# Performance work log

Measured on AMD Instinct MI355X. Metric: run time of the kernel, lower is better.

## Reference

```python
import jax, jax.numpy as jnp
import numpy as np

N = 50000      # nodes
E = 800000     # edges (avg degree 16)
IN = 512       # input features
OUT = 32       # per-head hidden features
H = 8          # heads (layer 1)
C = 16         # classes (layer 2, 1 head)
NEG_SLOPE = 0.2


def setup_inputs() -> dict:
    key = jax.random.key(0)
    ks = jax.random.split(key, 8)
    x = jax.random.normal(ks[0], (N, IN), jnp.float32)
    edge_index = jax.random.randint(ks[1], (2, E), 0, N, jnp.int32)
    # layer 1 params: W1 [IN, H*OUT], attention vectors a1_src/a1_dst [H, OUT]
    W1 = jax.random.normal(ks[2], (IN, H * OUT), jnp.float32) * (1.0 / np.sqrt(IN))
    a1_src = jax.random.normal(ks[3], (H, OUT), jnp.float32) * (1.0 / np.sqrt(OUT))
    a1_dst = jax.random.normal(ks[4], (H, OUT), jnp.float32) * (1.0 / np.sqrt(OUT))
    # layer 2 params: single head, W2 [H*OUT, C], a2_src/a2_dst [1, C]
    W2 = jax.random.normal(ks[5], (H * OUT, C), jnp.float32) * (1.0 / np.sqrt(H * OUT))
    a2_src = jax.random.normal(ks[6], (1, C), jnp.float32) * (1.0 / np.sqrt(C))
    a2_dst = jax.random.normal(ks[7], (1, C), jnp.float32) * (1.0 / np.sqrt(C))
    return {"x": x, "W1": W1, "a1_src": a1_src, "a1_dst": a1_dst,
            "W2": W2, "a2_src": a2_src, "a2_dst": a2_dst,
            "edge_index": edge_index}


def gat_layer(x, edge_index, W, a_src, a_dst, concat):
    """Standard GAT layer: e_ij = LeakyReLU(a_src.Wh_i + a_dst.Wh_j),
    softmax over incoming edges of each target node, scatter-aggregate."""
    n = x.shape[0]
    h_heads, f = a_src.shape
    h = (x @ W).reshape(n, h_heads, f)                      # [N, H, F]
    src, dst = edge_index[0], edge_index[1]
    es = jnp.einsum('nhf,hf->nh', h, a_src)                 # [N, H] per-node src scores
    ed = jnp.einsum('nhf,hf->nh', h, a_dst)                 # [N, H]
    e = jax.nn.leaky_relu(es[src] + ed[dst], NEG_SLOPE)     # [E, H] per-edge logits
    # segment softmax over edges grouped by dst node
    m = jax.ops.segment_max(e, dst, num_segments=n)         # [N, H]
    m = jnp.where(jnp.isfinite(m), m, 0.0)                  # empty segments -> -inf
    p = jnp.exp(e - m[dst])                                 # [E, H]
    s = jax.ops.segment_sum(p, dst, num_segments=n)         # [N, H]
    denom = s[dst]
    alpha = p / jnp.where(denom > 0, denom, 1.0)            # [E, H]
    msg = h[src] * alpha[:, :, None]                        # [E, H, F]
    out = jax.ops.segment_sum(msg, dst, num_segments=n)     # [N, H, F]
    if concat:
        return out.reshape(n, h_heads * f)
    return out.mean(axis=1)


def reference(x, W1, a1_src, a1_dst, W2, a2_src, a2_dst, edge_index):
    # dropout is identity in eval mode
    h = gat_layer(x, edge_index, W1, a1_src, a1_dst, concat=True)   # [N, H*OUT]
    h = jax.nn.elu(h)
    h = gat_layer(h, edge_index, W2, a2_src, a2_dst, concat=False)  # [N, C]
    return jax.nn.log_softmax(h, axis=1)
```

## Files before the change

kernel.cpp:

```cpp
#include <hip/hip_runtime.h>

#define NN 50000
#define EE 800000
#define KIN 512
#define HF 256
#define NH 8
#define FOUT 32
#define NC 16
#define NEG 0.2f
#define NB_SCAN 196

typedef unsigned short u16;
typedef __attribute__((ext_vector_type(8))) short shortx8;
typedef __attribute__((ext_vector_type(4))) float floatx4;
typedef __attribute__((ext_vector_type(8))) unsigned short ushortx8;
typedef __attribute__((ext_vector_type(4))) unsigned uintx4;

__device__ __forceinline__ float lrelu(float x) { return x > 0.f ? x : NEG * x; }

__device__ __forceinline__ u16 f2bf(float f) {
    unsigned u = __float_as_uint(f);
    return (u16)((u + 0x7FFFu + ((u >> 16) & 1u)) >> 16);
}
__device__ __forceinline__ float bf2f(u16 v) {
    return __uint_as_float((unsigned)v << 16);
}
__device__ __forceinline__ unsigned pk2bf(float a, float b) {
    unsigned ua = __float_as_uint(a), ub = __float_as_uint(b);
    return ((ua + 0x8000u) >> 16) | ((ub + 0x8000u) & 0xffff0000u);
}

__device__ __forceinline__ void gll16(const void* g, void* l) {
    __builtin_amdgcn_global_load_lds((const __attribute__((address_space(1))) void*)g,
                                     (__attribute__((address_space(3))) void*)l, 16, 0, 0);
}

__global__ void count_deg_convw(const int* __restrict__ dst, int* __restrict__ deg,
                                const float* __restrict__ W1, const float* __restrict__ W2,
                                u16* __restrict__ w1t, u16* __restrict__ w2t) {
    int e = blockIdx.x * 256 + threadIdx.x;
    if (e < EE) atomicAdd(&deg[dst[e]], 1);
    if (e < KIN * HF) {
        int k = e >> 8, n = e & 255;
        w1t[n * KIN + k] = f2bf(W1[e]);
    } else if (e < KIN * HF + HF * NC) {
        int e2 = e - KIN * HF;
        int k = e2 >> 4, c = e2 & 15;
        w2t[c * HF + k] = f2bf(W2[e2]);
    }
}

__global__ __launch_bounds__(256) void scan_a(const int* __restrict__ deg, int* __restrict__ bsum) {
    __shared__ int sm[256];
    int t = threadIdx.x;
    int i = blockIdx.x * 256 + t;
    sm[t] = (i < NN) ? deg[i] : 0;
    __syncthreads();
    for (int o = 128; o; o >>= 1) { if (t < o) sm[t] += sm[t + o]; __syncthreads(); }
    if (t == 0) bsum[blockIdx.x] = sm[0];
}

__global__ __launch_bounds__(256) void scan_c(const int* __restrict__ deg, const int* __restrict__ bsum,
                                              int* __restrict__ off) {
    __shared__ int sm[256];
    __shared__ int pre[256];
    int t = threadIdx.x;
    pre[t] = (t < blockIdx.x && t < NB_SCAN) ? bsum[t] : 0;
    __syncthreads();
    for (int o = 128; o; o >>= 1) { if (t < o) pre[t] += pre[t + o]; __syncthreads(); }
    int bofs = pre[0];
    __syncthreads();
    int i = blockIdx.x * 256 + t;
    int d = (i < NN) ? deg[i] : 0;
    sm[t] = d;
    __syncthreads();
    for (int dd = 1; dd < 256; dd <<= 1) {
        int v = (t >= dd) ? sm[t - dd] : 0;
        __syncthreads();
        sm[t] += v;
        __syncthreads();
    }
    if (i < NN) off[i] = bofs + sm[t] - d;
    if (i == 0) off[NN] = EE;
}

__global__ void fill_csr(const int* __restrict__ src, const int* __restrict__ dst,
                         const int* __restrict__ off, int* __restrict__ cursor,
                         int* __restrict__ csr_src) {
    int e = blockIdx.x * 256 + threadIdx.x;
    if (e < EE) {
        int d = dst[e];
        int pos = atomicAdd(&cursor[d], 1);
        csr_src[off[d] + pos] = src[e];
    }
}

__global__ __launch_bounds__(256, 3) void gemm1_mfma(const float* __restrict__ x,
                                                     const u16* __restrict__ w1t,
                                                     u16* __restrict__ h1b,
                                                     const float* __restrict__ a1s,
                                                     const float* __restrict__ a1d,
                                                     float* __restrict__ es1,
                                                     float* __restrict__ ed1) {
    __shared__ __align__(16) float As0[8 * 64 * 4];
    __shared__ __align__(16) float As1[8 * 64 * 4];
    __shared__ __align__(16) u16 Bs0[4 * 256 * 8];
    __shared__ __align__(16) u16 Bs1[4 * 256 * 8];
    int t = threadIdx.x;
    int lane = t & 63, wave = t >> 6;
    int wm = wave >> 1, wn = wave & 1;
    int lm = lane & 15, quad = lane >> 4;
    int bm = blockIdx.x * 64;

    floatx4 acc[2][8];
#pragma unroll
    for (int i = 0; i < 2; i++)
#pragma unroll
        for (int j = 0; j < 8; j++) acc[i][j] = (floatx4){0.f, 0.f, 0.f, 0.f};

    int arow = bm + lane;
    if (arow > NN - 1) arow = NN - 1;
    const float* axp = x + (size_t)arow * KIN;
    const u16* bxp[4];
#pragma unroll
    for (int b = 0; b < 4; b++) bxp[b] = w1t + (size_t)(b * 64 + lane) * KIN + wave * 8;

#define G1_STAGE(AB, BB, KK)                                             \
    {                                                                    \
        _Pragma("unroll") for (int a = 0; a < 2; a++) {                  \
            int g = wave * 2 + a;                                        \
            gll16(axp + (KK) + g * 4, &AB[g * 64 * 4]);                  \
        }                                                                \
        _Pragma("unroll") for (int b = 0; b < 4; b++)                    \
            gll16(bxp[b] + (KK), &BB[(wave * 256 + b * 64) * 8]);        \
    }

#define G1_WAITV(n) do { asm volatile("s_waitcnt vmcnt(" #n ")" ::: "memory"); \
                         __builtin_amdgcn_sched_barrier(0); } while (0)
#define G1_BAR() do { __builtin_amdgcn_sched_barrier(0);                 \
                      __builtin_amdgcn_s_barrier();                      \
                      __builtin_amdgcn_sched_barrier(0); } while (0)

#define G1_COMPUTE(AB, BB)                                               \
    {                                                                    \
        shortx8 af[2], bfv[8];                                           \
        _Pragma("unroll") for (int i = 0; i < 2; i++) {                  \
            int row = wm * 32 + i * 16 + lm;                             \
            int g0 = quad * 2;                                           \
            float4 lo = *(const float4*)&AB[(g0 * 64 + row) * 4];        \
            float4 hi = *(const float4*)&AB[((g0 + 1) * 64 + row) * 4];  \
            union { uintx4 u; shortx8 s; } cv;                           \
            cv.u[0] = pk2bf(lo.x, lo.y);                                 \
            cv.u[1] = pk2bf(lo.z, lo.w);                                 \
            cv.u[2] = pk2bf(hi.x, hi.y);                                 \
            cv.u[3] = pk2bf(hi.z, hi.w);                                 \
            af[i] = cv.s;                                                \
        }                                                                \
        _Pragma("unroll") for (int j = 0; j < 8; j++) {                  \
            int col = wn * 128 + j * 16 + lm;                            \
            bfv[j] = *(const shortx8*)&BB[(quad * 256 + col) * 8];       \
        }                                                                \
        _Pragma("unroll") for (int i = 0; i < 2; i++)                    \
            _Pragma("unroll") for (int j = 0; j < 8; j++)                \
                acc[i][j] = __builtin_amdgcn_mfma_f32_16x16x32_bf16(     \
                    af[i], bfv[j], acc[i][j], 0, 0, 0);                  \
    }

    G1_STAGE(As0, Bs0, 0);
#pragma unroll
    for (int it = 0; it < 16; ++it) {
        const int kk = it * 32;
        if (it < 15) {
            if (it & 1) { G1_STAGE(As0, Bs0, kk + 32); }
            else        { G1_STAGE(As1, Bs1, kk + 32); }
        }
        if (it < 15) { G1_WAITV(6); } else { G1_WAITV(0); }
        G1_BAR();
        if (it & 1) { G1_COMPUTE(As1, Bs1); }
        else        { G1_COMPUTE(As0, Bs0); }
        G1_BAR();
    }
#undef G1_STAGE
#undef G1_WAITV
#undef G1_BAR
#undef G1_COMPUTE

#pragma unroll
    for (int i = 0; i < 2; i++) {
        int row = bm + wm * 32 + i * 16 + quad * 4;
#pragma unroll
        for (int j = 0; j < 8; j++) {
            int col = wn * 128 + j * 16 + lm;
#pragma unroll
            for (int r = 0; r < 4; r++) {
                if (row + r < NN) h1b[(size_t)(row + r) * HF + col] = f2bf(acc[i][j][r]);
            }
        }
    }

    float as_v[8], ad_v[8];
#pragma unroll
    for (int j = 0; j < 8; j++) {
        int col = wn * 128 + j * 16 + lm;
        as_v[j] = a1s[col];
        ad_v[j] = a1d[col];
    }
#pragma unroll
    for (int i = 0; i < 2; i++) {
#pragma unroll
        for (int r = 0; r < 4; r++) {
            int row = bm + wm * 32 + i * 16 + quad * 4 + r;
#pragma unroll
            for (int hp = 0; hp < 4; hp++) {
                float e_s = acc[i][2 * hp][r] * as_v[2 * hp] + acc[i][2 * hp + 1][r] * as_v[2 * hp + 1];
                float e_d = acc[i][2 * hp][r] * ad_v[2 * hp] + acc[i][2 * hp + 1][r] * ad_v[2 * hp + 1];
#pragma unroll
                for (int o = 8; o; o >>= 1) {
                    e_s += __shfl_down(e_s, o, 16);
                    e_d += __shfl_down(e_d, o, 16);
                }
                if (lm == 0 && row < NN) {
                    int h = wn * 4 + hp;
                    es1[row * NH + h] = e_s;
                    ed1[row * NH + h] = e_d;
                }
            }
        }
    }
}

__global__ __launch_bounds__(256) void agg1_mfma(const u16* __restrict__ h1b, const float* __restrict__ es,
                                                 const float* __restrict__ ed, const int* __restrict__ off,
                                                 const int* __restrict__ csr_src, u16* __restrict__ out1b) {
    __shared__ __align__(16) u16 Hs[32 * 256];
    __shared__ __align__(16) u16 pTs[8][32];
    __shared__ __align__(16) unsigned char dstloc[32];
    __shared__ int offs_s[17];
    __shared__ float ed_s[16][8];

    int t = threadIdx.x;
    int lane = t & 63, wave = t >> 6;
    int lm = lane & 15, quad = lane >> 4;
    int base = blockIdx.x * 16;

    if (t < 17) offs_s[t] = off[base + t];
    if (t < 128) ed_s[t >> 3][t & 7] = ed[(base + (t >> 3)) * NH + (t & 7)];
    int e0 = off[base];
    int e1 = off[base + 16];
    int nch = (e1 - e0 + 31) >> 5;
    __syncthreads();

    floatx4 acc[2][2];
    floatx4 accS[2];
#pragma unroll
    for (int a = 0; a < 2; a++) {
        accS[a] = (floatx4){0.f, 0.f, 0.f, 0.f};
#pragma unroll
        for (int b = 0; b < 2; b++) acc[a][b] = (floatx4){0.f, 0.f, 0.f, 0.f};
    }

    int h0 = 2 * wave;
    shortx8 ones;
#pragma unroll
    for (int i = 0; i < 8; i++) ones[i] = (short)0x3F80;

    int k_p = t >> 3, h_p = t & 7;
    int sv = 0;
    if (nch > 0) {
        int g = e0 + (lane & 31);
        sv = csr_src[g < e1 ? g : e1 - 1];
    }

    for (int c = 0; c < nch; c++) {
        int svn = 0;
        if (c + 1 < nch) {
            int g = e0 + ((c + 1) << 5) + (lane & 31);
            svn = csr_src[g < e1 ? g : e1 - 1];
        }
#pragma unroll
        for (int pass = 0; pass < 4; pass++) {
            int r = pass * 8 + 2 * wave + (lane >> 5);
            int s = __shfl(sv, r, 64);
            const u16* sp = h1b + (size_t)s * HF + (((lane & 31) ^ (pass << 1)) << 3);
            gll16(sp, Hs + pass * 2048 + wave * 512);
        }
        {
            int g = e0 + (c << 5) + k_p;
            int s = __shfl(sv, k_p, 64);
            float pv = 0.f;
            if (g < e1) {
                int m = 0;
                if (offs_s[m + 8] <= g) m += 8;
                if (offs_s[m + 4] <= g) m += 4;
                if (offs_s[m + 2] <= g) m += 2;
                if (offs_s[m + 1] <= g) m += 1;
                float lg = es[s * NH + h_p] + ed_s[m][h_p];
                lg = lg > 0.f ? lg : NEG * lg;
                pv = __expf(lg);
                if (h_p == 0) dstloc[k_p] = (unsigned char)m;
            }
            pTs[h_p][k_p] = f2bf(pv);
        }
        __syncthreads();

        union { uintx4 u; shortx8 s; } pa, pb, a0, a1;
        pa.s = *(const shortx8*)&pTs[h0][quad * 8];
        pb.s = *(const shortx8*)&pTs[h0 + 1][quad * 8];
        unsigned dw0 = *(const unsigned*)&dstloc[quad * 8];
        unsigned dw1 = *(const unsigned*)&dstloc[quad * 8 + 4];
        unsigned ulm = (unsigned)lm;
        unsigned mm0 = ((dw0 & 255u) == ulm ? 0xffffu : 0u) | (((dw0 >> 8) & 255u) == ulm ? 0xffff0000u : 0u);
        unsigned mm1 = (((dw0 >> 16) & 255u) == ulm ? 0xffffu : 0u) | ((dw0 >> 24) == ulm ? 0xffff0000u : 0u);
        unsigned mm2 = ((dw1 & 255u) == ulm ? 0xffffu : 0u) | (((dw1 >> 8) & 255u) == ulm ? 0xffff0000u : 0u);
        unsigned mm3 = (((dw1 >> 16) & 255u) == ulm ? 0xffffu : 0u) | ((dw1 >> 24) == ulm ? 0xffff0000u : 0u);
        a0.u[0] = pa.u[0] & mm0; a0.u[1] = pa.u[1] & mm1; a0.u[2] = pa.u[2] & mm2; a0.u[3] = pa.u[3] & mm3;
        a1.u[0] = pb.u[0] & mm0; a1.u[1] = pb.u[1] & mm1; a1.u[2] = pb.u[2] & mm2; a1.u[3] = pb.u[3] & mm3;

        accS[0] = __builtin_amdgcn_mfma_f32_16x16x32_bf16(a0.s, ones, accS[0], 0, 0, 0);
        accS[1] = __builtin_amdgcn_mfma_f32_16x16x32_bf16(a1.s, ones, accS[1], 0, 0, 0);

#pragma unroll
        for (int hh = 0; hh < 2; hh++) {
#pragma unroll
            for (int half = 0; half < 2; half++) {
                int f = (h0 + hh) * 32 + half * 16 + lm;
                int bidx = (quad * 8) * 256 + (((f >> 3) ^ (quad << 1)) << 3) + (f & 7);
                shortx8 bfv;
#pragma unroll
                for (int j = 0; j < 8; j++) bfv[j] = (short)Hs[bidx + j * 256];
                acc[hh][half] = __builtin_amdgcn_mfma_f32_16x16x32_bf16(
                    hh ? a1.s : a0.s, bfv, acc[hh][half], 0, 0, 0);
            }
        }
        __syncthreads();
        sv = svn;
    }

#pragma unroll
    for (int hh = 0; hh < 2; hh++) {
#pragma unroll
        for (int r = 0; r < 4; r++) {
            float sden = accS[hh][r];
            float inv = sden > 0.f ? 1.0f / sden : 0.f;
            int n = base + quad * 4 + r;
#pragma unroll
            for (int half = 0; half < 2; half++) {
                float v = acc[hh][half][r] * inv;
                v = v > 0.f ? v : (__expf(v) - 1.0f);
                out1b[(size_t)n * HF + (h0 + hh) * 32 + half * 16 + lm] = f2bf(v);
            }
        }
    }
}

__global__ __launch_bounds__(64) void gemm2_mfma(const u16* __restrict__ out1b, const u16* __restrict__ w2t,
                                                 const float* __restrict__ a2s, const float* __restrict__ a2d,
                                                 u16* __restrict__ h2b, float* __restrict__ es2,
                                                 float* __restrict__ ed2) {
    int lane = threadIdx.x;
    int lm = lane & 15, quad = lane >> 4;
    int nb = blockIdx.x * 16;
    floatx4 acc = (floatx4){0.f, 0.f, 0.f, 0.f};
    const u16* arow = out1b + (size_t)(nb + lm) * HF + quad * 8;
    const u16* brow = w2t + lm * HF + quad * 8;
#pragma unroll
    for (int kk = 0; kk < HF; kk += 32) {
        shortx8 af = *(const shortx8*)(arow + kk);
        shortx8 bf = *(const shortx8*)(brow + kk);
        acc = __builtin_amdgcn_mfma_f32_16x16x32_bf16(af, bf, acc, 0, 0, 0);
    }
    float a2sc = a2s[lm], a2dc = a2d[lm];
#pragma unroll
    for (int r = 0; r < 4; r++) {
        int n = nb + quad * 4 + r;
        float v = acc[r];
        h2b[n * NC + lm] = f2bf(v);
        float ps = v * a2sc, pd = v * a2dc;
#pragma unroll
        for (int o = 8; o; o >>= 1) {
            ps += __shfl_down(ps, o, 16);
            pd += __shfl_down(pd, o, 16);
        }
        if (lm == 0) { es2[n] = ps; ed2[n] = pd; }
    }
}

__global__ __launch_bounds__(256) void agg2(const u16* __restrict__ h2b, const float* __restrict__ es2,
                                            const float* __restrict__ ed2, const int* __restrict__ off,
                                            const int* __restrict__ csr_src, float* __restrict__ out) {
    int t = threadIdx.x;
    int nid = blockIdx.x * 16 + (t >> 4);
    int c = t & 15;
    int beg = off[nid];
    int deg = off[nid + 1] - beg;
    float edn = ed2[nid];
    float s = 0.f, acc = 0.f;
    for (int base = 0; base < deg; base += 16) {
        int nch = deg - base; if (nch > 16) nch = 16;
        int sv = 0;
        if (c < nch) sv = csr_src[beg + base + c];
        int sva[16];
#pragma unroll
        for (int e = 0; e < 16; e++) sva[e] = __shfl(sv, e, 16);
        float hva[16];
#pragma unroll
        for (int e = 0; e < 16; e++) hva[e] = bf2f(h2b[sva[e] * NC + c]);
        float p = 0.f;
        if (c < nch) p = __expf(lrelu(es2[sv] + edn));
        s += p;
        float pa[16];
#pragma unroll
        for (int e = 0; e < 16; e++) pa[e] = __shfl(p, e, 16);
#pragma unroll
        for (int e = 0; e < 16; e++) acc += pa[e] * hva[e];
    }
#pragma unroll
    for (int o = 8; o; o >>= 1) s += __shfl_down(s, o, 16);
    s = __shfl(s, 0, 16);
    float v = (s > 0.f) ? acc / s : 0.f;
    float m2 = v;
#pragma unroll
    for (int o = 8; o; o >>= 1) m2 = fmaxf(m2, __shfl_down(m2, o, 16));
    m2 = __shfl(m2, 0, 16);
    float se = __expf(v - m2);
#pragma unroll
    for (int o = 8; o; o >>= 1) se += __shfl_down(se, o, 16);
    se = __shfl(se, 0, 16);
    out[nid * NC + c] = v - m2 - __logf(se);
}

extern "C" void kernel_launch(void* const* d_in, const int* in_sizes, int n_in,
                              void* d_out, int out_size, void* d_ws, size_t ws_size,
                              hipStream_t stream) {
    const float* x   = (const float*)d_in[0];
    const float* W1  = (const float*)d_in[1];
    const float* a1s = (const float*)d_in[2];
    const float* a1d = (const float*)d_in[3];
    const float* W2  = (const float*)d_in[4];
    const float* a2s = (const float*)d_in[5];
    const float* a2d = (const float*)d_in[6];
    const int*   ei  = (const int*)d_in[7];
    const int* srcv = ei;
    const int* dstv = ei + EE;
    float* out = (float*)d_out;

    u16* h1b    = (u16*)d_ws;
    u16* out1b  = h1b + (size_t)NN * HF;
    float* es1  = (float*)(out1b + (size_t)NN * HF);
    float* ed1  = es1 + (size_t)NN * NH;
    u16* h2b    = (u16*)(ed1 + (size_t)NN * NH);
    float* es2v = (float*)(h2b + (size_t)NN * NC);
    float* ed2v = es2v + NN;
    int* deg    = (int*)(ed2v + NN);
    int* cursor = deg + NN;
    int* offs   = cursor + NN;
    int* csr    = offs + NN + 1;
    int* bsum   = csr + EE;
    u16* w1t    = (u16*)(bsum + 256);
    u16* w2t    = w1t + (size_t)HF * KIN;

    hipMemsetAsync(deg, 0, 2 * NN * sizeof(int), stream);
    count_deg_convw<<<(EE + 255) / 256, 256, 0, stream>>>(dstv, deg, W1, W2, w1t, w2t);
    scan_a<<<NB_SCAN, 256, 0, stream>>>(deg, bsum);
    scan_c<<<NB_SCAN, 256, 0, stream>>>(deg, bsum, offs);
    fill_csr<<<(EE + 255) / 256, 256, 0, stream>>>(srcv, dstv, offs, cursor, csr);
    gemm1_mfma<<<(NN + 63) / 64, 256, 0, stream>>>(x, w1t, h1b, a1s, a1d, es1, ed1);
    agg1_mfma<<<NN / 16, 256, 0, stream>>>(h1b, es1, ed1, offs, csr, out1b);
    gemm2_mfma<<<NN / 16, 64, 0, stream>>>(out1b, w2t, a2s, a2d, h2b, es2v, ed2v);
    agg2<<<NN / 16, 256, 0, stream>>>(h2b, es2v, ed2v, offs, csr, out);
}
```

Baseline: 393.2 us.

## Pre-convert x and W1 to swizzled bf16 tiles before the layer-1 GEMM

The degree-count kernel now also converts x to bf16 and writes it into K-sliced, XOR-swizzled 64-row tiles. W1 is written the same way into swizzled per-K-slice tiles. The GEMM then loads bf16 tiles straight into LDS, with one A load per wave instead of two, and reads MFMA fragments without converting fp32 to bf16 and with fewer bank conflicts. In exchange, x is fully read once and written again as bf16 before the GEMM reads it back. The x buffer is aliased with out1b in the workspace to save memory.

```diff
diff --git a/kernel.cpp b/kernel.cpp
--- a/kernel.cpp
+++ b/kernel.cpp
@@ -9,6 +9,7 @@
 #define NC 16
 #define NEG 0.2f
 #define NB_SCAN 196
+#define NP 50048
 
 typedef unsigned short u16;
 typedef __attribute__((ext_vector_type(8))) short shortx8;
@@ -36,15 +37,47 @@
 }
 
 __global__ void count_deg_convw(const int* __restrict__ dst, int* __restrict__ deg,
-                                const float* __restrict__ W1, const float* __restrict__ W2,
-                                u16* __restrict__ w1t, u16* __restrict__ w2t) {
+                                const float* __restrict__ x, const float* __restrict__ W1,
+                                const float* __restrict__ W2,
+                                u16* __restrict__ xb2, u16* __restrict__ w1t2,
+                                u16* __restrict__ w2t) {
     int e = blockIdx.x * 256 + threadIdx.x;
-    if (e < EE) atomicAdd(&deg[dst[e]], 1);
-    if (e < KIN * HF) {
-        int k = e >> 8, n = e & 255;
-        w1t[n * KIN + k] = f2bf(W1[e]);
-    } else if (e < KIN * HF + HF * NC) {
-        int e2 = e - KIN * HF;
+    if (e < EE) {
+        atomicAdd(&deg[dst[e]], 1);
+        int n = e >> 4, ks = e & 15;
+        const float* xr = x + (size_t)n * KIN + ks * 32;
+        u16* tile = xb2 + ((size_t)ks * NP + (size_t)(n & ~63)) * 32;
+        int r = n & 63;
+#pragma unroll
+        for (int g = 0; g < 4; g++) {
+            float4 lo = *(const float4*)(xr + g * 8);
+            float4 hi = *(const float4*)(xr + g * 8 + 4);
+            uintx4 v;
+            v[0] = pk2bf(lo.x, lo.y);
+            v[1] = pk2bf(lo.z, lo.w);
+            v[2] = pk2bf(hi.x, hi.y);
+            v[3] = pk2bf(hi.z, hi.w);
+            unsigned bo = (unsigned)((r * 64 + g * 16) ^ ((r & 7) << 4));
+            *(uintx4*)((char*)tile + bo) = v;
+        }
+    } else if (e < EE + 16 * 256) {
+        int i = e - EE;
+        int ks = i >> 8, col = i & 255;
+        u16* tile = w1t2 + (size_t)ks * 8192;
+#pragma unroll
+        for (int g = 0; g < 4; g++) {
+            uintx4 v;
+#pragma unroll
+            for (int p = 0; p < 4; p++) {
+                u16 a = f2bf(W1[(size_t)(ks * 32 + g * 8 + 2 * p) * HF + col]);
+                u16 b = f2bf(W1[(size_t)(ks * 32 + g * 8 + 2 * p + 1) * HF + col]);
+                v[p] = (unsigned)a | ((unsigned)b << 16);
+            }
+            unsigned bo = (unsigned)((col * 64 + g * 16) ^ ((col & 7) << 4));
+            *(uintx4*)((char*)tile + bo) = v;
+        }
+    } else if (e < EE + 16 * 256 + HF * NC) {
+        int e2 = e - EE - 16 * 256;
         int k = e2 >> 4, c = e2 & 15;
         w2t[c * HF + k] = f2bf(W2[e2]);
     }
@@ -95,17 +128,17 @@
     }
 }
 
-__global__ __launch_bounds__(256, 3) void gemm1_mfma(const float* __restrict__ x,
-                                                     const u16* __restrict__ w1t,
+__global__ __launch_bounds__(256, 3) void gemm1_mfma(const u16* __restrict__ xb2,
+                                                     const u16* __restrict__ w1t2,
                                                      u16* __restrict__ h1b,
                                                      const float* __restrict__ a1s,
                                                      const float* __restrict__ a1d,
                                                      float* __restrict__ es1,
                                                      float* __restrict__ ed1) {
-    __shared__ __align__(16) float As0[8 * 64 * 4];
-    __shared__ __align__(16) float As1[8 * 64 * 4];
-    __shared__ __align__(16) u16 Bs0[4 * 256 * 8];
-    __shared__ __align__(16) u16 Bs1[4 * 256 * 8];
+    __shared__ __align__(16) u16 As0[2048];
+    __shared__ __align__(16) u16 As1[2048];
+    __shared__ __align__(16) u16 Bs0[8192];
+    __shared__ __align__(16) u16 Bs1[8192];
     int t = threadIdx.x;
     int lane = t & 63, wave = t >> 6;
     int wm = wave >> 1, wn = wave & 1;
@@ -118,21 +151,15 @@
 #pragma unroll
         for (int j = 0; j < 8; j++) acc[i][j] = (floatx4){0.f, 0.f, 0.f, 0.f};
 
-    int arow = bm + lane;
-    if (arow > NN - 1) arow = NN - 1;
-    const float* axp = x + (size_t)arow * KIN;
-    const u16* bxp[4];
-#pragma unroll
-    for (int b = 0; b < 4; b++) bxp[b] = w1t + (size_t)(b * 64 + lane) * KIN + wave * 8;
-
-#define G1_STAGE(AB, BB, KK)                                             \
+    const u16* abase = xb2 + (size_t)bm * 32 + wave * 512 + lane * 8;
+    const u16* bbase = w1t2 + lane * 8;
+
+#define G1_STAGE(AB, BB, KS)                                             \
     {                                                                    \
-        _Pragma("unroll") for (int a = 0; a < 2; a++) {                  \
-            int g = wave * 2 + a;                                        \
-            gll16(axp + (KK) + g * 4, &AB[g * 64 * 4]);                  \
-        }                                                                \
+        gll16(abase + (size_t)(KS) * (NP * 32), AB + wave * 512);        \
         _Pragma("unroll") for (int b = 0; b < 4; b++)                    \
-            gll16(bxp[b] + (KK), &BB[(wave * 256 + b * 64) * 8]);        \
+            gll16(bbase + (KS) * 8192 + (wave * 4 + b) * 512,            \
+                  BB + (wave * 4 + b) * 512);                            \
     }
 
 #define G1_WAITV(n) do { asm volatile("s_waitcnt vmcnt(" #n ")" ::: "memory"); \
@@ -146,19 +173,13 @@
         shortx8 af[2], bfv[8];                                           \
         _Pragma("unroll") for (int i = 0; i < 2; i++) {                  \
             int row = wm * 32 + i * 16 + lm;                             \
-            int g0 = quad * 2;                                           \
-            float4 lo = *(const float4*)&AB[(g0 * 64 + row) * 4];        \
-            float4 hi = *(const float4*)&AB[((g0 + 1) * 64 + row) * 4];  \
-            union { uintx4 u; shortx8 s; } cv;                           \
-            cv.u[0] = pk2bf(lo.x, lo.y);                                 \
-            cv.u[1] = pk2bf(lo.z, lo.w);                                 \
-            cv.u[2] = pk2bf(hi.x, hi.y);                                 \
-            cv.u[3] = pk2bf(hi.z, hi.w);                                 \
-            af[i] = cv.s;                                                \
+            unsigned bo = (unsigned)((row * 64 + quad * 16) ^ ((row & 7) << 4)); \
+            af[i] = *(const shortx8*)((const char*)AB + bo);             \
         }                                                                \
         _Pragma("unroll") for (int j = 0; j < 8; j++) {                  \
             int col = wn * 128 + j * 16 + lm;                            \
-            bfv[j] = *(const shortx8*)&BB[(quad * 256 + col) * 8];       \
+            unsigned bo = (unsigned)((col * 64 + quad * 16) ^ ((col & 7) << 4)); \
+            bfv[j] = *(const shortx8*)((const char*)BB + bo);            \
         }                                                                \
         _Pragma("unroll") for (int i = 0; i < 2; i++)                    \
             _Pragma("unroll") for (int j = 0; j < 8; j++)                \
@@ -169,12 +190,11 @@
     G1_STAGE(As0, Bs0, 0);
 #pragma unroll
     for (int it = 0; it < 16; ++it) {
-        const int kk = it * 32;
         if (it < 15) {
-            if (it & 1) { G1_STAGE(As0, Bs0, kk + 32); }
-            else        { G1_STAGE(As1, Bs1, kk + 32); }
-        }
-        if (it < 15) { G1_WAITV(6); } else { G1_WAITV(0); }
+            if (it & 1) { G1_STAGE(As0, Bs0, it + 1); }
+            else        { G1_STAGE(As1, Bs1, it + 1); }
+        }
+        if (it < 15) { G1_WAITV(5); } else { G1_WAITV(0); }
         G1_BAR();
         if (it & 1) { G1_COMPUTE(As1, Bs1); }
         else        { G1_COMPUTE(As0, Bs0); }
@@ -444,27 +464,30 @@
     const int* dstv = ei + EE;
     float* out = (float*)d_out;
 
-    u16* h1b    = (u16*)d_ws;
-    u16* out1b  = h1b + (size_t)NN * HF;
-    float* es1  = (float*)(out1b + (size_t)NN * HF);
-    float* ed1  = es1 + (size_t)NN * NH;
-    u16* h2b    = (u16*)(ed1 + (size_t)NN * NH);
+    char* W = (char*)d_ws;
+    u16* h1b    = (u16*)W;  W += (size_t)NN * HF * 2;
+    float* es1  = (float*)W; W += (size_t)NN * NH * 4;
+    float* ed1  = (float*)W; W += (size_t)NN * NH * 4;
+    int* csr    = (int*)W;  W += (size_t)EE * 4;
+    int* bsum   = (int*)W;  W += 1024;
+    u16* w1t2   = (u16*)W;  W += (size_t)16 * 256 * 32 * 2;
+    u16* w2t    = (u16*)W;  W += (size_t)NC * HF * 2;
+    int* deg    = (int*)W;  W += (size_t)NN * 4;
+    int* cursor = (int*)W;  W += (size_t)NN * 4;
+    int* offs   = (int*)W;  W += 200064;
+    u16* xb2    = (u16*)W;
+    u16* out1b  = (u16*)W;
+    u16* h2b    = out1b + (size_t)NN * HF;
     float* es2v = (float*)(h2b + (size_t)NN * NC);
     float* ed2v = es2v + NN;
-    int* deg    = (int*)(ed2v + NN);
-    int* cursor = deg + NN;
-    int* offs   = cursor + NN;
-    int* csr    = offs + NN + 1;
-    int* bsum   = csr + EE;
-    u16* w1t    = (u16*)(bsum + 256);
-    u16* w2t    = w1t + (size_t)HF * KIN;
 
     hipMemsetAsync(deg, 0, 2 * NN * sizeof(int), stream);
-    count_deg_convw<<<(EE + 255) / 256, 256, 0, stream>>>(dstv, deg, W1, W2, w1t, w2t);
+    count_deg_convw<<<(EE + 16 * 256 + HF * NC + 255) / 256, 256, 0, stream>>>(
+        dstv, deg, x, W1, W2, xb2, w1t2, w2t);
     scan_a<<<NB_SCAN, 256, 0, stream>>>(deg, bsum);
     scan_c<<<NB_SCAN, 256, 0, stream>>>(deg, bsum, offs);
     fill_csr<<<(EE + 255) / 256, 256, 0, stream>>>(srcv, dstv, offs, cursor, csr);
-    gemm1_mfma<<<(NN + 63) / 64, 256, 0, stream>>>(x, w1t, h1b, a1s, a1d, es1, ed1);
+    gemm1_mfma<<<(NN + 63) / 64, 256, 0, stream>>>(xb2, w1t2, h1b, a1s, a1d, es1, ed1);
     agg1_mfma<<<NN / 16, 256, 0, stream>>>(h1b, es1, ed1, offs, csr, out1b);
     gemm2_mfma<<<NN / 16, 64, 0, stream>>>(out1b, w2t, a2s, a2d, h2b, es2v, ed2v);
     agg2<<<NN / 16, 256, 0, stream>>>(h2b, es2v, ed2v, offs, csr, out);
```

Measured after the change: 361.5 us. -8.1%, faster.
